# Kernel optimization log

Hardware: AMD Instinct MI355X
Metric: run time of the kernel (lower is better)

## Reference

```python
import jax, jax.numpy as jnp
import numpy as np

NUM_HEADS = 16

def setup_inputs() -> dict:
    key = jax.random.key(0)
    k1, k2, k3 = jax.random.split(key, 3)
    B, S, D = 2, 2048, 1024
    return {
        "hidden_states": jax.random.normal(k1, (B, S, D), dtype=jnp.float32),
        "W_attn": jax.random.normal(k2, (D, 3 * D), dtype=jnp.float32) * 0.02,
        "b_attn": jnp.zeros((3 * D,), dtype=jnp.float32),
        "W_proj": jax.random.normal(k3, (D, D), dtype=jnp.float32) * 0.02,
        "b_proj": jnp.zeros((D,), dtype=jnp.float32),
    }

def reference(hidden_states, W_attn, b_attn, W_proj, b_proj):
    B, S, D = hidden_states.shape
    H = NUM_HEADS
    hd = D // H
    # qkv projection (Conv1D == addmm): [B,S,3D]
    qkv = hidden_states @ W_attn + b_attn
    q, k, v = jnp.split(qkv, 3, axis=-1)
    # split heads -> [B,H,S,hd]
    def split_heads(t):
        return t.reshape(B, S, H, hd).transpose(0, 2, 1, 3)
    q, k, v = split_heads(q), split_heads(k), split_heads(v)
    # scaled QK^T: [B,H,S,S]
    scores = jnp.einsum('bhqd,bhkd->bhqk', q, k) / jnp.asarray(hd ** 0.5, dtype=q.dtype)
    causal = jnp.tril(jnp.ones((S, S), dtype=bool))
    mask_value = jnp.finfo(scores.dtype).min
    scores = jnp.where(causal, scores, mask_value)
    probs = jax.nn.softmax(scores, axis=-1)  # attn_pdrop=0 -> no dropout
    out = jnp.einsum('bhqk,bhkd->bhqd', probs, v)
    # merge heads -> [B,S,D]
    out = out.transpose(0, 2, 1, 3).reshape(B, S, D)
    out = out @ W_proj + b_proj  # resid_pdrop=0 -> no dropout
    return out
```

## Files before the change

kernel.cpp:

```cpp
#include <hip/hip_runtime.h>
#include <math.h>

typedef __attribute__((ext_vector_type(8))) short bf16x8;
typedef __attribute__((ext_vector_type(4))) short bf16x4;
typedef __attribute__((ext_vector_type(4))) float f32x4;

#define MFMA16(a, b, c) __builtin_amdgcn_mfma_f32_16x16x32_bf16(a, b, c, 0, 0, 0)

#define GLOAD_LDS16(g, l)                                                        \
    __builtin_amdgcn_global_load_lds(                                            \
        (const __attribute__((address_space(1))) void*)(g),                      \
        (__attribute__((address_space(3))) void*)(l), 16, 0, 0)

__device__ __forceinline__ short f2bf(float f) {
    union { float f; unsigned u; } x; x.f = f;
    unsigned r = (x.u + 0x7fffu + ((x.u >> 16) & 1u)) >> 16;
    return (short)r;
}

__global__ __launch_bounds__(256) void convert_bf16_kernel(
    const float* __restrict__ in, short* __restrict__ out, int n4) {
    int i = blockIdx.x * 256 + threadIdx.x;
    if (i >= n4) return;
    float4 v = ((const float4*)in)[i];
    bf16x4 o;
    o[0] = f2bf(v.x); o[1] = f2bf(v.y); o[2] = f2bf(v.z); o[3] = f2bf(v.w);
    ((bf16x4*)out)[i] = o;
}

__global__ __launch_bounds__(256) void transpose_w2_kernel(
    const float* __restrict__ Wa, const float* __restrict__ Wp,
    short* __restrict__ WaT, short* __restrict__ WpT) {
    __shared__ float tile[32][33];
    const float* W; short* Wt; int N, xb;
    if (blockIdx.x < 96) { W = Wa; Wt = WaT; N = 3072; xb = blockIdx.x; }
    else                 { W = Wp; Wt = WpT; N = 1024; xb = blockIdx.x - 96; }
    const int K = 1024;
    int c = threadIdx.x & 31, r0 = threadIdx.x >> 5;
    int n0 = xb << 5, k0 = blockIdx.y << 5;
#pragma unroll
    for (int i = 0; i < 4; i++) {
        int r = r0 + i * 8;
        tile[r][c] = W[(long)(k0 + r) * N + n0 + c];
    }
    __syncthreads();
#pragma unroll
    for (int i = 0; i < 4; i++) {
        int r = r0 + i * 8;
        Wt[(long)(n0 + r) * K + k0 + c] = f2bf(tile[c][r]);
    }
}

__global__ __launch_bounds__(256) void gemm_qkv_kernel(
    const short* __restrict__ A, const short* __restrict__ Bt,
    const float* __restrict__ bias,
    short* __restrict__ QK, short* __restrict__ VTb, int Kdim) {
    __shared__ __align__(16) short lsAll[17408];
    short* lsA = lsAll;
    short* lsB = lsAll + 8192;
    const int tid = threadIdx.x;
    const int lane = tid & 63, l15 = lane & 15, quad = lane >> 4;
    const int w = tid >> 6, wm = w >> 1, wn = w & 1;
    const int m0 = blockIdx.y * 128, n0 = blockIdx.x * 128;
    const int e = l15 & 7;
    const int lrow = lane >> 3;
    const int lgcol = ((lane & 7) ^ lrow) << 3;

    f32x4 acc[4][4];
#pragma unroll
    for (int i = 0; i < 4; i++)
#pragma unroll
        for (int j = 0; j < 4; j++) acc[i][j] = (f32x4){0.f, 0.f, 0.f, 0.f};

    for (int k0 = 0; k0 < Kdim; k0 += 64) {
#pragma unroll
        for (int ii = 0; ii < 4; ii++) {
            const int i = (w << 2) + ii;
            const int grow = (i << 3) + lrow;
            GLOAD_LDS16(&A[(size_t)(m0 + grow) * Kdim + k0 + lgcol], &lsA[i * 512]);
            GLOAD_LDS16(&Bt[(size_t)(n0 + grow) * Kdim + k0 + lgcol], &lsB[i * 512]);
        }
        __syncthreads();
#pragma unroll
        for (int kk = 0; kk < 64; kk += 32) {
            const int kb = kk >> 3;
            bf16x8 af[4], bfr[4];
#pragma unroll
            for (int t = 0; t < 4; t++) {
                const int sw = (((kb + quad) ^ e) << 3);
                af[t] = *(const bf16x8*)&lsA[(wm * 64 + t * 16 + l15) * 64 + sw];
                bfr[t] = *(const bf16x8*)&lsB[(wn * 64 + t * 16 + l15) * 64 + sw];
            }
#pragma unroll
            for (int mt = 0; mt < 4; mt++)
#pragma unroll
                for (int nt = 0; nt < 4; nt++)
                    acc[mt][nt] = MFMA16(af[mt], bfr[nt], acc[mt][nt]);
        }
        __syncthreads();
    }

    if (n0 < 2048) {
        const float scale = (n0 < 1024) ? 0.18033688011112042f : 1.0f;
#pragma unroll
        for (int nt = 0; nt < 4; nt++) {
            int nn = n0 + wn * 64 + nt * 16 + l15;
            float bv = bias[nn];
#pragma unroll
            for (int mt = 0; mt < 4; mt++)
#pragma unroll
                for (int r = 0; r < 4; r++) {
                    int mm = m0 + wm * 64 + mt * 16 + quad * 4 + r;
                    QK[(long)mm * 2048 + nn] = f2bf((acc[mt][nt][r] + bv) * scale);
                }
        }
    } else {
        short* vt = &lsAll[w * (64 * 68)];
#pragma unroll
        for (int nt = 0; nt < 4; nt++) {
            int nn = n0 + wn * 64 + nt * 16 + l15;
            float bv = bias[nn];
#pragma unroll
            for (int mt = 0; mt < 4; mt++) {
                bf16x4 pk;
#pragma unroll
                for (int r = 0; r < 4; r++) pk[r] = f2bf(acc[mt][nt][r] + bv);
                *(bf16x4*)&vt[(nt * 16 + l15) * 68 + mt * 16 + quad * 4] = pk;
            }
        }
        const int hh = ((n0 - 2048) >> 6) + wn;
        const int bb = m0 >> 11;
        const int srow = (m0 & 2047) + wm * 64;
        const int sloc = (lane & 7) << 3;
#pragma unroll
        for (int i = 0; i < 8; i++) {
            const int d = i * 8 + (lane >> 3);
            bf16x8 vv = *(const bf16x8*)&vt[d * 68 + sloc];
            *(bf16x8*)&VTb[((size_t)(bb * 16 + hh) * 64 + d) * 2048 + srow + sloc] = vv;
        }
    }
}

__global__ __launch_bounds__(256) void gemm_proj_kernel(
    const short* __restrict__ A, const short* __restrict__ Bt,
    const float* __restrict__ bias, float* __restrict__ outF) {
    __shared__ __align__(16) short lsA[128 * 64];
    __shared__ __align__(16) short lsB[64 * 64];
    const int tid = threadIdx.x;
    const int lane = tid & 63, l15 = lane & 15, quad = lane >> 4, w = tid >> 6;
    const int m0 = blockIdx.y * 128, n0 = blockIdx.x * 64;
    const int e = l15 & 7;
    const int lrow = lane >> 3;
    const int lgcol = ((lane & 7) ^ lrow) << 3;

    f32x4 acc[2][4];
#pragma unroll
    for (int i = 0; i < 2; i++)
#pragma unroll
        for (int j = 0; j < 4; j++) acc[i][j] = (f32x4){0.f, 0.f, 0.f, 0.f};

    for (int k0 = 0; k0 < 1024; k0 += 64) {
#pragma unroll
        for (int ii = 0; ii < 4; ii++) {
            const int i = (w << 2) + ii;
            const int grow = (i << 3) + lrow;
            GLOAD_LDS16(&A[(size_t)(m0 + grow) * 1024 + k0 + lgcol], &lsA[i * 512]);
        }
#pragma unroll
        for (int ii = 0; ii < 2; ii++) {
            const int i = (w << 1) + ii;
            const int grow = (i << 3) + lrow;
            GLOAD_LDS16(&Bt[(size_t)(n0 + grow) * 1024 + k0 + lgcol], &lsB[i * 512]);
        }
        __syncthreads();
#pragma unroll
        for (int kk = 0; kk < 64; kk += 32) {
            const int kb = kk >> 3;
            const int sw = (((kb + quad) ^ e) << 3);
            bf16x8 af[2], bfr[4];
#pragma unroll
            for (int mt = 0; mt < 2; mt++)
                af[mt] = *(const bf16x8*)&lsA[(w * 32 + mt * 16 + l15) * 64 + sw];
#pragma unroll
            for (int nt = 0; nt < 4; nt++)
                bfr[nt] = *(const bf16x8*)&lsB[(nt * 16 + l15) * 64 + sw];
#pragma unroll
            for (int mt = 0; mt < 2; mt++)
#pragma unroll
                for (int nt = 0; nt < 4; nt++)
                    acc[mt][nt] = MFMA16(af[mt], bfr[nt], acc[mt][nt]);
        }
        __syncthreads();
    }

#pragma unroll
    for (int nt = 0; nt < 4; nt++) {
        int nn = n0 + nt * 16 + l15;
        float bv = bias[nn];
#pragma unroll
        for (int mt = 0; mt < 2; mt++)
#pragma unroll
            for (int r = 0; r < 4; r++) {
                int mm = m0 + w * 32 + mt * 16 + quad * 4 + r;
                outF[(long)mm * 1024 + nn] = acc[mt][nt][r] + bv;
            }
    }
}

__global__ __launch_bounds__(256, 4) void attn_kernel(
    const short* __restrict__ QK, const short* __restrict__ VT,
    short* __restrict__ Ao) {
    __shared__ __align__(16) short Kt[2][64 * 64];
    __shared__ __align__(16) short Vt[2][64 * 64];
    __shared__ __align__(16) short Pt[4][1024];
    const int tid = threadIdx.x;
    const int lane = tid & 63, l15 = lane & 15, quad = lane >> 4, w = tid >> 6;
    const int bx = blockIdx.x;
    const int qt = 31 - (bx >> 5);
    const int hb = bx & 31;
    const int b = hb >> 4, h = hb & 15;
    const size_t rowbase = (size_t)b * 2048 * 2048 + h * 64;
    const short* Qb = QK + rowbase;
    const short* Kb = QK + rowbase + 1024;
    const short* Vh = VT + (size_t)hb * 64 * 2048;
    short* Pw = &Pt[w][0];
    const int e = l15 & 7;

    const int srow0 = tid >> 3, sc40 = (tid & 7) ^ (srow0 & 7);
    const int srow1 = srow0 + 32, sc41 = (tid & 7) ^ (srow1 & 7);
    const int sdst0 = srow0 * 64 + ((tid & 7) << 3);
    const int sdst1 = srow1 * 64 + ((tid & 7) << 3);

    const long qr = (long)(qt * 64 + w * 16 + l15) * 2048;
    bf16x8 qf0 = *(const bf16x8*)&Qb[qr + quad * 8];
    bf16x8 qf1 = *(const bf16x8*)&Qb[qr + 32 + quad * 8];

    float l = 0.f;
    f32x4 o[4];
#pragma unroll
    for (int dt = 0; dt < 4; dt++) o[dt] = (f32x4){0.f, 0.f, 0.f, 0.f};

    const int nc = qt + 1;

    *(bf16x8*)&Kt[0][sdst0] = *(const bf16x8*)&Kb[(size_t)srow0 * 2048 + sc40 * 8];
    *(bf16x8*)&Kt[0][sdst1] = *(const bf16x8*)&Kb[(size_t)srow1 * 2048 + sc41 * 8];
    *(bf16x8*)&Vt[0][sdst0] = *(const bf16x8*)&Vh[srow0 * 2048 + sc40 * 8];
    *(bf16x8*)&Vt[0][sdst1] = *(const bf16x8*)&Vh[srow1 * 2048 + sc41 * 8];
    __syncthreads();

    for (int c = 0; c < nc; c++) {
        const short* Kc = &Kt[c & 1][0];
        const short* Vc = &Vt[c & 1][0];
        const bool more = (c + 1 < nc);
        bf16x8 kr0, kr1, vr0, vr1;
        if (more) {
            const int k2 = (c + 1) * 64;
            kr0 = *(const bf16x8*)&Kb[(size_t)(k2 + srow0) * 2048 + sc40 * 8];
            kr1 = *(const bf16x8*)&Kb[(size_t)(k2 + srow1) * 2048 + sc41 * 8];
            vr0 = *(const bf16x8*)&Vh[srow0 * 2048 + k2 + sc40 * 8];
            vr1 = *(const bf16x8*)&Vh[srow1 * 2048 + k2 + sc41 * 8];
        }

        f32x4 s[4];
#pragma unroll
        for (int t = 0; t < 4; t++) {
            bf16x8 k0f = *(const bf16x8*)&Kc[(t * 16 + l15) * 64 + ((quad ^ e) << 3)];
            bf16x8 k1f = *(const bf16x8*)&Kc[(t * 16 + l15) * 64 + (((4 + quad) ^ e) << 3)];
            f32x4 z = (f32x4){0.f, 0.f, 0.f, 0.f};
            z = MFMA16(k0f, qf0, z);
            z = MFMA16(k1f, qf1, z);
            s[t] = z;
        }

        if (c == nc - 1) {
#pragma unroll
            for (int t = 0; t < 4; t++)
#pragma unroll
                for (int r = 0; r < 4; r++)
                    if (t * 16 + quad * 4 + r > w * 16 + l15) s[t][r] = -INFINITY;
        }

#pragma unroll
        for (int t = 0; t < 4; t++) {
            bf16x4 pw;
#pragma unroll
            for (int r = 0; r < 4; r++) {
                float pv = __builtin_amdgcn_exp2f(s[t][r]);
                l += pv;
                pw[r] = f2bf(pv);
            }
            *(bf16x4*)&Pw[l15 * 64 + (((2 * t + (quad >> 1)) ^ e) << 3) + ((quad & 1) << 2)] = pw;
        }

        bf16x8 pf0 = *(const bf16x8*)&Pw[l15 * 64 + ((quad ^ e) << 3)];
        bf16x8 pf1 = *(const bf16x8*)&Pw[l15 * 64 + (((4 + quad) ^ e) << 3)];
#pragma unroll
        for (int dt = 0; dt < 4; dt++) {
            bf16x8 v0f = *(const bf16x8*)&Vc[(dt * 16 + l15) * 64 + ((quad ^ e) << 3)];
            bf16x8 v1f = *(const bf16x8*)&Vc[(dt * 16 + l15) * 64 + (((4 + quad) ^ e) << 3)];
            o[dt] = MFMA16(v0f, pf0, o[dt]);
            o[dt] = MFMA16(v1f, pf1, o[dt]);
        }

        if (more) {
            short* Kn = &Kt[(c + 1) & 1][0];
            short* Vn = &Vt[(c + 1) & 1][0];
            *(bf16x8*)&Kn[sdst0] = kr0;
            *(bf16x8*)&Kn[sdst1] = kr1;
            *(bf16x8*)&Vn[sdst0] = vr0;
            *(bf16x8*)&Vn[sdst1] = vr1;
        }
        __syncthreads();
    }

    l += __shfl_xor(l, 16);
    l += __shfl_xor(l, 32);
    const float rl = 1.f / l;

    const int qs = qt * 64 + w * 16 + l15;
    const long base = ((long)(b * 2048 + qs)) * 1024 + h * 64;
#pragma unroll
    for (int dt = 0; dt < 4; dt++) {
        bf16x4 wv;
#pragma unroll
        for (int r = 0; r < 4; r++) wv[r] = f2bf(o[dt][r] * rl);
        *(bf16x4*)&Ao[base + dt * 16 + quad * 4] = wv;
    }
}

extern "C" void kernel_launch(void* const* d_in, const int* in_sizes, int n_in,
                              void* d_out, int out_size, void* d_ws, size_t ws_size,
                              hipStream_t stream) {
    const float* hs = (const float*)d_in[0];
    const float* W_attn = (const float*)d_in[1];
    const float* b_attn = (const float*)d_in[2];
    const float* W_proj = (const float*)d_in[3];
    const float* b_proj = (const float*)d_in[4];
    float* out = (float*)d_out;

    const size_t MB = 1024 * 1024;
    char* ws = (char*)d_ws;
    short* hs_bf = (short*)ws;
    short* attn_o = hs_bf;
    short* WaT = (short*)(ws + 8 * MB);
    short* WpT = (short*)(ws + 14 * MB);
    short* QK = (short*)(ws + 16 * MB);
    short* VTb = (short*)(ws + 32 * MB);

    convert_bf16_kernel<<<4096, 256, 0, stream>>>(hs, hs_bf, 1048576);
    transpose_w2_kernel<<<dim3(128, 32), 256, 0, stream>>>(W_attn, W_proj, WaT, WpT);
    gemm_qkv_kernel<<<dim3(24, 32), 256, 0, stream>>>(hs_bf, WaT, b_attn, QK, VTb, 1024);
    attn_kernel<<<1024, 256, 0, stream>>>(QK, VTb, attn_o);
    gemm_proj_kernel<<<dim3(16, 32), 256, 0, stream>>>(attn_o, WpT, b_proj, out);
}
```

Baseline: 183.6 us.

## Merge prep kernels and load V fragments directly from global memory

Merges the hidden-state bf16 conversion and the weight transpose into one prep launch, saving a kernel launch. In attention, V tiles are no longer staged through double-buffered shared memory. Each lane loads its V MFMA fragments straight from global (L2) memory every iteration. This halves the LDS footprint, which may allow more blocks per CU, and removes LDS writes and reads for V. The cost is per-iteration global load latency that is not prefetched a stage ahead, plus some redundant global traffic across waves.

Measured after the change: 226.4 us. 23.3% more time.

```diff
diff --git a/kernel.cpp b/kernel.cpp
--- a/kernel.cpp
+++ b/kernel.cpp
@@ -18,26 +18,28 @@
     return (short)r;
 }
 
-__global__ __launch_bounds__(256) void convert_bf16_kernel(
-    const float* __restrict__ in, short* __restrict__ out, int n4) {
-    int i = blockIdx.x * 256 + threadIdx.x;
-    if (i >= n4) return;
-    float4 v = ((const float4*)in)[i];
-    bf16x4 o;
-    o[0] = f2bf(v.x); o[1] = f2bf(v.y); o[2] = f2bf(v.z); o[3] = f2bf(v.w);
-    ((bf16x4*)out)[i] = o;
-}
-
-__global__ __launch_bounds__(256) void transpose_w2_kernel(
+__global__ __launch_bounds__(256) void prep_kernel(
+    const float* __restrict__ hs, short* __restrict__ hs_bf,
     const float* __restrict__ Wa, const float* __restrict__ Wp,
     short* __restrict__ WaT, short* __restrict__ WpT) {
     __shared__ float tile[32][33];
+    const int bx = blockIdx.x;
+    if (bx < 4096) {
+        int i = bx * 256 + threadIdx.x;
+        float4 v = ((const float4*)hs)[i];
+        bf16x4 o;
+        o[0] = f2bf(v.x); o[1] = f2bf(v.y); o[2] = f2bf(v.z); o[3] = f2bf(v.w);
+        ((bf16x4*)hs_bf)[i] = o;
+        return;
+    }
+    const int idx = bx - 4096;
     const float* W; short* Wt; int N, xb;
-    if (blockIdx.x < 96) { W = Wa; Wt = WaT; N = 3072; xb = blockIdx.x; }
-    else                 { W = Wp; Wt = WpT; N = 1024; xb = blockIdx.x - 96; }
+    const int xraw = idx & 127, ky = idx >> 7;
+    if (xraw < 96) { W = Wa; Wt = WaT; N = 3072; xb = xraw; }
+    else           { W = Wp; Wt = WpT; N = 1024; xb = xraw - 96; }
     const int K = 1024;
     int c = threadIdx.x & 31, r0 = threadIdx.x >> 5;
-    int n0 = xb << 5, k0 = blockIdx.y << 5;
+    int n0 = xb << 5, k0 = ky << 5;
 #pragma unroll
     for (int i = 0; i < 4; i++) {
         int r = r0 + i * 8;
@@ -211,7 +213,6 @@
     const short* __restrict__ QK, const short* __restrict__ VT,
     short* __restrict__ Ao) {
     __shared__ __align__(16) short Kt[2][64 * 64];
-    __shared__ __align__(16) short Vt[2][64 * 64];
     __shared__ __align__(16) short Pt[4][1024];
     const int tid = threadIdx.x;
     const int lane = tid & 63, l15 = lane & 15, quad = lane >> 4, w = tid >> 6;
@@ -244,21 +245,25 @@
 
     *(bf16x8*)&Kt[0][sdst0] = *(const bf16x8*)&Kb[(size_t)srow0 * 2048 + sc40 * 8];
     *(bf16x8*)&Kt[0][sdst1] = *(const bf16x8*)&Kb[(size_t)srow1 * 2048 + sc41 * 8];
-    *(bf16x8*)&Vt[0][sdst0] = *(const bf16x8*)&Vh[srow0 * 2048 + sc40 * 8];
-    *(bf16x8*)&Vt[0][sdst1] = *(const bf16x8*)&Vh[srow1 * 2048 + sc41 * 8];
     __syncthreads();
 
     for (int c = 0; c < nc; c++) {
         const short* Kc = &Kt[c & 1][0];
-        const short* Vc = &Vt[c & 1][0];
+        const int kt = c * 64;
         const bool more = (c + 1 < nc);
-        bf16x8 kr0, kr1, vr0, vr1;
+        bf16x8 kr0, kr1;
         if (more) {
-            const int k2 = (c + 1) * 64;
+            const int k2 = kt + 64;
             kr0 = *(const bf16x8*)&Kb[(size_t)(k2 + srow0) * 2048 + sc40 * 8];
             kr1 = *(const bf16x8*)&Kb[(size_t)(k2 + srow1) * 2048 + sc41 * 8];
-            vr0 = *(const bf16x8*)&Vh[srow0 * 2048 + k2 + sc40 * 8];
-            vr1 = *(const bf16x8*)&Vh[srow1 * 2048 + k2 + sc41 * 8];
+        }
+
+        bf16x8 v0f[4], v1f[4];
+#pragma unroll
+        for (int dt = 0; dt < 4; dt++) {
+            const short* vrow = &Vh[(dt * 16 + l15) * 2048 + kt];
+            v0f[dt] = *(const bf16x8*)&vrow[quad * 8];
+            v1f[dt] = *(const bf16x8*)&vrow[32 + quad * 8];
         }
 
         f32x4 s[4];
@@ -296,19 +301,14 @@
         bf16x8 pf1 = *(const bf16x8*)&Pw[l15 * 64 + (((4 + quad) ^ e) << 3)];
 #pragma unroll
         for (int dt = 0; dt < 4; dt++) {
-            bf16x8 v0f = *(const bf16x8*)&Vc[(dt * 16 + l15) * 64 + ((quad ^ e) << 3)];
-            bf16x8 v1f = *(const bf16x8*)&Vc[(dt * 16 + l15) * 64 + (((4 + quad) ^ e) << 3)];
-            o[dt] = MFMA16(v0f, pf0, o[dt]);
-            o[dt] = MFMA16(v1f, pf1, o[dt]);
+            o[dt] = MFMA16(v0f[dt], pf0, o[dt]);
+            o[dt] = MFMA16(v1f[dt], pf1, o[dt]);
         }
 
         if (more) {
             short* Kn = &Kt[(c + 1) & 1][0];
-            short* Vn = &Vt[(c + 1) & 1][0];
             *(bf16x8*)&Kn[sdst0] = kr0;
             *(bf16x8*)&Kn[sdst1] = kr1;
-            *(bf16x8*)&Vn[sdst0] = vr0;
-            *(bf16x8*)&Vn[sdst1] = vr1;
         }
         __syncthreads();
     }
@@ -347,8 +347,7 @@
     short* QK = (short*)(ws + 16 * MB);
     short* VTb = (short*)(ws + 32 * MB);
 
-    convert_bf16_kernel<<<4096, 256, 0, stream>>>(hs, hs_bf, 1048576);
-    transpose_w2_kernel<<<dim3(128, 32), 256, 0, stream>>>(W_attn, W_proj, WaT, WpT);
+    prep_kernel<<<8192, 256, 0, stream>>>(hs, hs_bf, W_attn, W_proj, WaT, WpT);
     gemm_qkv_kernel<<<dim3(24, 32), 256, 0, stream>>>(hs_bf, WaT, b_attn, QK, VTb, 1024);
     attn_kernel<<<1024, 256, 0, stream>>>(QK, VTb, attn_o);
     gemm_proj_kernel<<<dim3(16, 32), 256, 0, stream>>>(attn_o, WpT, b_proj, out);
```
